# Kernel tuning notes

Hardware: AMD Instinct MI355X
Metric: run time of the kernel (lower is better)

## Reference

```python
import jax, jax.numpy as jnp
import numpy as np

H, I = 16, 64
SCALE = 1.0 / (I ** 0.5)

def _rel_shift(x):
    # x: (S, J, B, H) -> Transformer-XL relative shift trick
    S, J, B, Hh = x.shape
    pad = jnp.zeros((S, 1, B, Hh), dtype=x.dtype)
    y = jnp.concatenate([pad, x], axis=1)           # (S, J+1, B, H)
    y = y.reshape(J + 1, S, B, Hh)[1:]              # (J, S, B, H)
    return y.reshape(S, J, B, Hh)

def setup_inputs() -> dict:
    key = jax.random.key(0)
    ks = jax.random.split(key, 10)
    S, P, B, E = 1024, 1024, 4, 1024
    J = P + S
    # causal mask: query s may attend keys j <= P + s; True = blocked
    mask = (jnp.arange(J)[None, :] > (P + jnp.arange(S))[:, None])[..., None]  # (S,J,1) bool
    sc = E ** -0.5
    return {
        "inputMHA": jax.random.normal(ks[0], (S, B, E), jnp.float32),
        "posEmbeddings": jax.random.normal(ks[1], (J, E), jnp.float32),
        "memory": jax.random.normal(ks[2], (P, B, E), jnp.float32),
        "u": jax.random.normal(ks[3], (H, I), jnp.float32) * 0.02,
        "v": jax.random.normal(ks[4], (H, I), jnp.float32) * 0.02,
        "mask": mask,
        "W_kv": jax.random.normal(ks[5], (E, 2 * H * I), jnp.float32) * sc,
        "W_q": jax.random.normal(ks[6], (E, H * I), jnp.float32) * sc,
        "W_p": jax.random.normal(ks[7], (E, H * I), jnp.float32) * sc,
        "W_o": jax.random.normal(ks[8], (H * I, E), jnp.float32) * sc,
        "gamma": jnp.ones((E,), jnp.float32),
        "beta": jnp.zeros((E,), jnp.float32),
    }

def reference(inputMHA, posEmbeddings, memory, u, v, mask, W_kv, W_q, W_p, W_o, gamma, beta):
    S, B, E = inputMHA.shape
    P = memory.shape[0]
    J = P + S
    x = jnp.concatenate([memory, inputMHA], axis=0)          # (J,B,E)
    kv = x @ W_kv                                            # (J,B,2HI)
    keys, values = jnp.split(kv, 2, axis=-1)
    q = (inputMHA @ W_q).reshape(S, B, H, I)                 # (S,B,H,I)
    K = keys.reshape(J, B, H, I)
    content = jnp.einsum('sbhi,jbhi->sjbh', q + u, K)        # content score
    p = (posEmbeddings @ W_p).reshape(J, H, I)               # (J,H,I)
    pos = jnp.einsum('sbhi,jhi->sjbh', q + v, p)             # position score
    pos = _rel_shift(pos)
    attn = content + pos                                     # (S,J,B,H)
    attn = jnp.where(mask[..., None], -jnp.inf, attn)        # mask (S,J,1)->(S,J,1,1)
    attn = jax.nn.softmax(attn * jnp.asarray(SCALE, attn.dtype), axis=1)
    V = values.reshape(J, B, H, I)
    awv = jnp.einsum('sjbh,jbhi->sbhi', attn, V).reshape(S, B, H * I)
    out = inputMHA + awv @ W_o                               # residual (dropout = eval identity)
    mean = jnp.mean(out, axis=-1, keepdims=True)
    var = jnp.var(out, axis=-1, keepdims=True)
    return (out - mean) / jnp.sqrt(var + 1e-5) * gamma + beta
```

## Files before the change

### kernel.cpp

```cpp
#include <hip/hip_runtime.h>
#include <hip/hip_bf16.h>

#define S_ 1024
#define P_ 1024
#define B_ 4
#define E_ 1024
#define J_ 2048
#define H_ 16
#define I_ 64

typedef __bf16 bf16_t;
typedef __bf16 bf16x8 __attribute__((ext_vector_type(8)));
typedef __bf16 bf16x4 __attribute__((ext_vector_type(4)));
typedef unsigned short u16x8 __attribute__((ext_vector_type(8)));
typedef float f32x4 __attribute__((ext_vector_type(4)));

#define MFMA16(a, b, c) __builtin_amdgcn_mfma_f32_16x16x32_bf16(a, b, c, 0, 0, 0)

#define SWZ(r, c) (((r) << 6) + ((((((c) >> 3)) ^ ((r) & 7)) << 3)) + ((c) & 7))

__global__ __launch_bounds__(256) void cvt_all_kernel(const float* __restrict__ memory,
                                                      const float* __restrict__ input,
                                                      const float* __restrict__ posEmb,
                                                      bf16_t* __restrict__ Xbf,
                                                      bf16_t* __restrict__ Pemb) {
    int blk = blockIdx.x;
    const float* src;
    bf16_t* dst;
    if (blk < 4096) { src = memory; dst = Xbf; }
    else if (blk < 8192) { blk -= 4096; src = input; dst = Xbf + (size_t)P_ * B_ * E_; }
    else { blk -= 8192; src = posEmb; dst = Pemb; }
    int i = (blk * 256 + threadIdx.x) * 4;
    float4 v = *(const float4*)(src + i);
    bf16x4 o = {(bf16_t)v.x, (bf16_t)v.y, (bf16_t)v.z, (bf16_t)v.w};
    *(bf16x4*)(dst + i) = o;
}

__global__ void trans_all_kernel(const float* __restrict__ W_kv, bf16_t* __restrict__ Wkvt,
                                 const float* __restrict__ W_q, bf16_t* __restrict__ Wqt,
                                 const float* __restrict__ W_p, bf16_t* __restrict__ Wpt,
                                 const float* __restrict__ W_o, bf16_t* __restrict__ Wot) {
    __shared__ float tile[32][33];
    int z = blockIdx.z;
    const float* W = (z == 0) ? W_kv : (z == 1) ? W_q : (z == 2) ? W_p : W_o;
    bf16_t* Wt = (z == 0) ? Wkvt : (z == 1) ? Wqt : (z == 2) ? Wpt : Wot;
    int N = (z == 0) ? 2048 : 1024;
    if (blockIdx.x * 32 >= N) return;
    int n0 = blockIdx.x * 32, k0 = blockIdx.y * 32;
    int x = threadIdx.x, y = threadIdx.y;
    for (int i = 0; i < 32; i += 8)
        tile[y + i][x] = W[(size_t)(k0 + y + i) * N + n0 + x];
    __syncthreads();
    for (int i = 0; i < 32; i += 8)
        Wt[(size_t)(n0 + y + i) * 1024 + k0 + x] = (bf16_t)tile[x][y + i];
}

__device__ __forceinline__ void gemm_tile(
    const bf16_t* __restrict__ A, const bf16_t* __restrict__ Bt, int N,
    int m0, int n0, int epi,
    bf16_t* __restrict__ out0, bf16_t* __restrict__ out1,
    const float* __restrict__ add0, const float* __restrict__ add1,
    float* __restrict__ outf,
    bf16_t (*Al)[72], bf16_t (*Bl)[72]) {
    const int K = 1024;
    int tid = threadIdx.x;
    int wave = tid >> 6, lane = tid & 63, quad = lane >> 4, l16 = lane & 15;
    int wm = (wave & 1) * 64, wn = (wave >> 1) * 64;
    f32x4 zero = {0.f, 0.f, 0.f, 0.f};
    f32x4 acc[4][4];
    #pragma unroll
    for (int i = 0; i < 4; i++)
        #pragma unroll
        for (int j = 0; j < 4; j++) acc[i][j] = zero;

    for (int k0 = 0; k0 < K; k0 += 64) {
        __syncthreads();
        #pragma unroll
        for (int r = 0; r < 4; r++) {
            int idx = tid + 256 * r;
            int row = idx >> 3, seg = (idx & 7) * 8;
            *(uint4*)&Al[row][seg] = *(const uint4*)&A[(size_t)(m0 + row) * K + k0 + seg];
            *(uint4*)&Bl[row][seg] = *(const uint4*)&Bt[(size_t)(n0 + row) * K + k0 + seg];
        }
        __syncthreads();
        #pragma unroll
        for (int ks = 0; ks < 2; ks++) {
            bf16x8 af[4], bfr[4];
            #pragma unroll
            for (int i = 0; i < 4; i++)
                af[i] = *(const bf16x8*)&Al[wm + i * 16 + l16][ks * 32 + quad * 8];
            #pragma unroll
            for (int j = 0; j < 4; j++)
                bfr[j] = *(const bf16x8*)&Bl[wn + j * 16 + l16][ks * 32 + quad * 8];
            #pragma unroll
            for (int i = 0; i < 4; i++)
                #pragma unroll
                for (int j = 0; j < 4; j++) acc[i][j] = MFMA16(af[i], bfr[j], acc[i][j]);
        }
    }
    #pragma unroll
    for (int i = 0; i < 4; i++)
        #pragma unroll
        for (int j = 0; j < 4; j++)
            #pragma unroll
            for (int reg = 0; reg < 4; reg++) {
                int m = m0 + wm + i * 16 + quad * 4 + reg;
                int n = n0 + wn + j * 16 + l16;
                float v = acc[i][j][reg];
                if (epi == 0) {
                    out0[(size_t)m * N + n] = (bf16_t)v;
                } else if (epi == 1) {
                    out0[(size_t)m * N + n] = (bf16_t)(v + add0[n]);
                    out1[(size_t)m * N + n] = (bf16_t)(v + add1[n]);
                } else {
                    outf[(size_t)m * N + n] = v + add0[(size_t)m * N + n];
                }
            }
}

__global__ __launch_bounds__(256) void gemm3_kernel(
    const bf16_t* __restrict__ Xbf, const bf16_t* __restrict__ Wkvt, bf16_t* __restrict__ kvb,
    const bf16_t* __restrict__ Wqt, bf16_t* __restrict__ qub, bf16_t* __restrict__ qvb,
    const float* __restrict__ u, const float* __restrict__ v,
    const bf16_t* __restrict__ Pemb, const bf16_t* __restrict__ Wpt, bf16_t* __restrict__ pb) {
    __shared__ __attribute__((aligned(16))) bf16_t Al[128][72];
    __shared__ __attribute__((aligned(16))) bf16_t Bl[128][72];
    int id = blockIdx.x;
    if (id < 1024) {
        gemm_tile(Xbf, Wkvt, 2048, (id >> 4) * 128, (id & 15) * 128, 0,
                  kvb, nullptr, nullptr, nullptr, nullptr, Al, Bl);
    } else if (id < 1280) {
        int t = id - 1024;
        gemm_tile(Xbf + (size_t)P_ * B_ * E_, Wqt, 1024, (t >> 3) * 128, (t & 7) * 128, 1,
                  qub, qvb, u, v, nullptr, Al, Bl);
    } else {
        int t = id - 1280;
        gemm_tile(Pemb, Wpt, 1024, (t >> 3) * 128, (t & 7) * 128, 0,
                  pb, nullptr, nullptr, nullptr, nullptr, Al, Bl);
    }
}

__global__ __launch_bounds__(256) void gemmo_kernel(
    const bf16_t* __restrict__ awvb, const bf16_t* __restrict__ Wot,
    const float* __restrict__ inputMHA, float* __restrict__ opre) {
    __shared__ __attribute__((aligned(16))) bf16_t Al[128][72];
    __shared__ __attribute__((aligned(16))) bf16_t Bl[128][72];
    int id = blockIdx.x;
    gemm_tile(awvb, Wot, 1024, (id >> 3) * 128, (id & 7) * 128, 2,
              nullptr, nullptr, inputMHA, nullptr, opre, Al, Bl);
}

__global__ __launch_bounds__(256) void flash_kernel(
    const bf16_t* __restrict__ qu, const bf16_t* __restrict__ qv,
    const bf16_t* __restrict__ kv, const bf16_t* __restrict__ pm,
    float* __restrict__ Oacc, float* __restrict__ lacc) {
    __shared__ __attribute__((aligned(16))) bf16_t Klds[64 * 64];
    __shared__ __attribute__((aligned(16))) bf16_t Vt[64 * 64];
    __shared__ __attribute__((aligned(16))) bf16_t Plds[128 * 64];
    __shared__ __attribute__((aligned(16))) bf16_t Prob[4 * 16 * 64];

    int tid = threadIdx.x;
    int wave = tid >> 6, lane = tid & 63, quad = lane >> 4, l16 = lane & 15;

    int x = blockIdx.x;
    int s_blk, c;
    if (x < 24) { s_blk = x / 3; c = x - s_blk * 3; }
    else        { int y = x - 24; s_blk = 8 + (y >> 2); c = y & 3; }
    int nt = 17 + s_blk;
    int t0 = c * 8;
    int t1 = t0 + 8; if (t1 > nt) t1 = nt;

    int s0 = s_blk * 64;
    int bh = blockIdx.y;
    int b = bh >> 4, h = bh & 15;
    int srow0 = s0 + wave * 16;

    const bf16_t* qub = qu + ((size_t)(srow0 + l16) * B_ + b) * 1024 + h * 64 + quad * 8;
    const bf16_t* qvb = qv + ((size_t)(srow0 + l16) * B_ + b) * 1024 + h * 64 + quad * 8;
    bf16x8 aqu0 = *(const bf16x8*)(qub);
    bf16x8 aqu1 = *(const bf16x8*)(qub + 32);
    bf16x8 aqv0 = *(const bf16x8*)(qvb);
    bf16x8 aqv1 = *(const bf16x8*)(qvb + 32);

    f32x4 zero = {0.f, 0.f, 0.f, 0.f};
    f32x4 accO[4];
    #pragma unroll
    for (int ot = 0; ot < 4; ot++) accO[ot] = zero;
    float lrowp[4] = {0.f, 0.f, 0.f, 0.f};

    const int w0u = 960 - s0;
    const int woff = 48 - wave * 16;
    const float SCL = 0.125f * 1.44269504088896f;

    int jr = tid >> 3, seg8g = tid & 7;
    int jp = tid & 31, iseg = tid >> 5;
    uint* VtU = (uint*)&Vt[0];
    bf16_t* ProbW = Prob + (wave << 10);

    {
        int j0 = t0 * 64;
        const bf16_t* kp = kv + ((size_t)(j0 + jr) * B_ + b) * 2048 + h * 64 + seg8g * 8;
        uint4 ka = *(const uint4*)kp;
        uint4 kb = *(const uint4*)(kp + (size_t)32 * B_ * 2048);
        const bf16_t* vp = kv + ((size_t)(j0 + jp * 2) * B_ + b) * 2048 + 1024 + h * 64 + iseg * 8;
        u16x8 va = *(const u16x8*)vp;
        u16x8 vb = *(const u16x8*)(vp + (size_t)B_ * 2048);
        uint4 pd[4];
        #pragma unroll
        for (int r = 0; r < 4; r++) {
            int idx = tid + 256 * r;
            int pr = idx >> 3, pg = idx & 7;
            int lr = w0u + j0 + pr; if (lr > J_ - 1) lr = J_ - 1;
            pd[r] = *(const uint4*)(pm + (size_t)lr * 1024 + h * 64 + pg * 8);
        }
        *(uint4*)&Klds[SWZ(jr, seg8g * 8)] = ka;
        *(uint4*)&Klds[SWZ(jr + 32, seg8g * 8)] = kb;
        #pragma unroll
        for (int e = 0; e < 8; e++) {
            int row = iseg * 8 + e;
            VtU[(row << 5) + ((((jp >> 2) ^ (row & 7)) << 2)) + (jp & 3)] =
                (uint)va[e] | ((uint)vb[e] << 16);
        }
        #pragma unroll
        for (int r = 0; r < 4; r++) {
            int idx = tid + 256 * r;
            int pr = idx >> 3, pg = idx & 7;
            *(uint4*)&Plds[SWZ((w0u + j0 + pr) & 127, pg * 8)] = pd[r];
        }
    }
    __syncthreads();

    for (int it = t0; it < t1; it++) {
        int j0 = it * 64;
        bool pf = (it + 1 < t1);
        uint4 ka, kb, pd0, pd1;
        u16x8 va, vb;
        int pr0 = tid >> 3, pg0 = tid & 7;
        int pr1 = (tid + 256) >> 3, pg1 = tid & 7;
        if (pf) {
            int j1 = j0 + 64;
            const bf16_t* kp = kv + ((size_t)(j1 + jr) * B_ + b) * 2048 + h * 64 + seg8g * 8;
            ka = *(const uint4*)kp;
            kb = *(const uint4*)(kp + (size_t)32 * B_ * 2048);
            const bf16_t* vp = kv + ((size_t)(j1 + jp * 2) * B_ + b) * 2048 + 1024 + h * 64 + iseg * 8;
            va = *(const u16x8*)vp;
            vb = *(const u16x8*)(vp + (size_t)B_ * 2048);
            int lr0 = w0u + j0 + 128 + pr0; if (lr0 > J_ - 1) lr0 = J_ - 1;
            int lr1 = w0u + j0 + 128 + pr1; if (lr1 > J_ - 1) lr1 = J_ - 1;
            pd0 = *(const uint4*)(pm + (size_t)lr0 * 1024 + h * 64 + pg0 * 8);
            pd1 = *(const uint4*)(pm + (size_t)lr1 * 1024 + h * 64 + pg1 * 8);
        }

        f32x4 cs[4];
        #pragma unroll
        for (int t = 0; t < 4; t++) cs[t] = zero;
        #pragma unroll
        for (int ks = 0; ks < 2; ks++) {
            bf16x8 aq = ks ? aqu1 : aqu0;
            #pragma unroll
            for (int t = 0; t < 4; t++) {
                bf16x8 bk = *(const bf16x8*)&Klds[SWZ(t * 16 + l16, ks * 32 + quad * 8)];
                cs[t] = MFMA16(aq, bk, cs[t]);
            }
        }
        f32x4 ep[5];
        #pragma unroll
        for (int t = 0; t < 5; t++) ep[t] = zero;
        #pragma unroll
        for (int ks = 0; ks < 2; ks++) {
            bf16x8 aq = ks ? aqv1 : aqv0;
            #pragma unroll
            for (int t = 0; t < 5; t++) {
                int prow = (w0u + j0 + woff + t * 16 + l16) & 127;
                bf16x8 bp = *(const bf16x8*)&Plds[SWZ(prow, ks * 32 + quad * 8)];
                ep[t] = MFMA16(aq, bp, ep[t]);
            }
        }

        #pragma unroll
        for (int reg = 0; reg < 4; reg++) {
            int r = quad * 4 + reg;
            int s = srow0 + r;
            int idx = l16 + 15 - r;
            int srcl = quad * 16 + (idx & 15);
            float sh[5];
            #pragma unroll
            for (int t = 0; t < 5; t++) sh[t] = __shfl(ep[t][reg], srcl);
            float psum = 0.f;
            #pragma unroll
            for (int t = 0; t < 4; t++) {
                float pos = (idx < 16) ? sh[t] : sh[t + 1];
                float p = exp2f((cs[t][reg] + pos) * SCL);
                p = (j0 + t * 16 + l16 > P_ + s) ? 0.f : p;
                ProbW[SWZ(r, t * 16 + l16)] = (bf16_t)p;
                psum += p;
            }
            lrowp[reg] += psum;
        }

        #pragma unroll
        for (int ks = 0; ks < 2; ks++) {
            bf16x8 pa = *(const bf16x8*)&Prob[(wave << 10) + SWZ(l16, ks * 32 + quad * 8)];
            #pragma unroll
            for (int ot = 0; ot < 4; ot++) {
                bf16x8 bv = *(const bf16x8*)&Vt[SWZ(ot * 16 + l16, ks * 32 + quad * 8)];
                accO[ot] = MFMA16(pa, bv, accO[ot]);
            }
        }

        __syncthreads();
        if (pf) {
            *(uint4*)&Klds[SWZ(jr, seg8g * 8)] = ka;
            *(uint4*)&Klds[SWZ(jr + 32, seg8g * 8)] = kb;
            #pragma unroll
            for (int e2 = 0; e2 < 8; e2++) {
                int row = iseg * 8 + e2;
                VtU[(row << 5) + ((((jp >> 2) ^ (row & 7)) << 2)) + (jp & 3)] =
                    (uint)va[e2] | ((uint)vb[e2] << 16);
            }
            *(uint4*)&Plds[SWZ((w0u + j0 + pr0) & 127, pg0 * 8)] = pd0;
            *(uint4*)&Plds[SWZ((w0u + j0 + pr1) & 127, pg1 * 8)] = pd1;
        }
        __syncthreads();
    }

    #pragma unroll
    for (int reg = 0; reg < 4; reg++) {
        int r = quad * 4 + reg;
        int srow = srow0 + r;
        float l = lrowp[reg];
        #pragma unroll
        for (int d = 1; d < 16; d <<= 1) l += __shfl_xor(l, d);
        if (l16 == 0) atomicAdd(&lacc[((size_t)srow * B_ + b) * H_ + h], l);
        size_t rowoff = ((size_t)srow * B_ + b) * 1024 + h * 64;
        #pragma unroll
        for (int ot = 0; ot < 4; ot++)
            atomicAdd(&Oacc[rowoff + ot * 16 + l16], accO[ot][reg]);
    }
}

__global__ __launch_bounds__(256) void norm_kernel(const float* __restrict__ Oacc,
                                                   const float* __restrict__ lacc,
                                                   bf16_t* __restrict__ awv) {
    int i4 = (blockIdx.x * 256 + threadIdx.x) * 4;
    int row = i4 >> 6;
    float inv = 1.0f / lacc[row];
    float4 o = *(const float4*)(Oacc + i4);
    bf16x4 r = {(bf16_t)(o.x * inv), (bf16_t)(o.y * inv),
                (bf16_t)(o.z * inv), (bf16_t)(o.w * inv)};
    *(bf16x4*)(awv + i4) = r;
}

__global__ __launch_bounds__(256) void ln_kernel(const float* __restrict__ x,
                                                 const float* __restrict__ gamma,
                                                 const float* __restrict__ beta,
                                                 float* __restrict__ out) {
    int row = blockIdx.x, tid = threadIdx.x;
    int lane = tid & 63, wave = tid >> 6;
    float4 v = ((const float4*)(x + (size_t)row * 1024))[tid];
    float s = v.x + v.y + v.z + v.w;
    float ss = v.x * v.x + v.y * v.y + v.z * v.z + v.w * v.w;
    #pragma unroll
    for (int sh = 1; sh < 64; sh <<= 1) { s += __shfl_xor(s, sh); ss += __shfl_xor(ss, sh); }
    __shared__ float red[8];
    if (lane == 0) { red[wave] = s; red[4 + wave] = ss; }
    __syncthreads();
    s = red[0] + red[1] + red[2] + red[3];
    ss = red[4] + red[5] + red[6] + red[7];
    float mean = s * (1.f / 1024.f);
    float var = ss * (1.f / 1024.f) - mean * mean;
    float inv = rsqrtf(var + 1e-5f);
    float4 g = ((const float4*)gamma)[tid];
    float4 bt = ((const float4*)beta)[tid];
    float4 o;
    o.x = (v.x - mean) * inv * g.x + bt.x;
    o.y = (v.y - mean) * inv * g.y + bt.y;
    o.z = (v.z - mean) * inv * g.z + bt.z;
    o.w = (v.w - mean) * inv * g.w + bt.w;
    ((float4*)(out + (size_t)row * 1024))[tid] = o;
}

extern "C" void kernel_launch(void* const* d_in, const int* in_sizes, int n_in,
                              void* d_out, int out_size, void* d_ws, size_t ws_size,
                              hipStream_t stream) {
    const float* inputMHA = (const float*)d_in[0];
    const float* posEmb   = (const float*)d_in[1];
    const float* memory   = (const float*)d_in[2];
    const float* u        = (const float*)d_in[3];
    const float* v        = (const float*)d_in[4];
    const float* W_kv     = (const float*)d_in[6];
    const float* W_q      = (const float*)d_in[7];
    const float* W_p      = (const float*)d_in[8];
    const float* W_o      = (const float*)d_in[9];
    const float* gamma    = (const float*)d_in[10];
    const float* beta     = (const float*)d_in[11];
    float* out = (float*)d_out;

    char* ws = (char*)d_ws;
    size_t off = 0;
    auto alloc = [&](size_t bytes) -> void* {
        void* p = ws + off;
        off += (bytes + 255) & ~(size_t)255;
        return p;
    };
    bf16_t* Xbf  = (bf16_t*)alloc((size_t)J_ * B_ * E_ * 2);
    bf16_t* Wkvt = (bf16_t*)alloc((size_t)2048 * 1024 * 2);
    bf16_t* Wqt  = (bf16_t*)alloc((size_t)1024 * 1024 * 2);
    bf16_t* Wpt  = (bf16_t*)alloc((size_t)1024 * 1024 * 2);
    bf16_t* Wot  = (bf16_t*)alloc((size_t)1024 * 1024 * 2);
    bf16_t* Pemb = (bf16_t*)alloc((size_t)2048 * 1024 * 2);
    bf16_t* kvb  = (bf16_t*)alloc((size_t)8192 * 2048 * 2);
    bf16_t* qub  = (bf16_t*)alloc((size_t)4096 * 1024 * 2);
    bf16_t* qvb  = (bf16_t*)alloc((size_t)4096 * 1024 * 2);
    bf16_t* pb   = (bf16_t*)alloc((size_t)2048 * 1024 * 2);
    bf16_t* awvb = (bf16_t*)alloc((size_t)4096 * 1024 * 2);
    float*  opre = (float*)alloc((size_t)4096 * 1024 * 4);
    float*  Oacc = (float*)alloc((size_t)4096 * 1024 * 4);
    float*  lacc = (float*)alloc((size_t)S_ * B_ * H_ * 4);

    hipMemsetAsync(Oacc, 0, (size_t)4096 * 1024 * 4, stream);
    hipMemsetAsync(lacc, 0, (size_t)S_ * B_ * H_ * 4, stream);

    cvt_all_kernel<<<10240, 256, 0, stream>>>(memory, inputMHA, posEmb, Xbf, Pemb);
    trans_all_kernel<<<dim3(64, 32, 4), dim3(32, 8), 0, stream>>>(
        W_kv, Wkvt, W_q, Wqt, W_p, Wpt, W_o, Wot);

    gemm3_kernel<<<1408, 256, 0, stream>>>(Xbf, Wkvt, kvb, Wqt, qub, qvb, u, v, Pemb, Wpt, pb);

    flash_kernel<<<dim3(56, B_ * H_), 256, 0, stream>>>(qub, qvb, kvb, pb, Oacc, lacc);
    norm_kernel<<<4096, 256, 0, stream>>>(Oacc, lacc, awvb);

    gemmo_kernel<<<256, 256, 0, stream>>>(awvb, Wot, inputMHA, opre);
    ln_kernel<<<S_ * B_, 256, 0, stream>>>(opre, gamma, beta, out);
}
```

Baseline: 444.5 us.

## Precompute relative-shifted position scores in a separate kernel before flash attention

Adds a pos_kernel that computes the (q+v)·p position scores for all query/key tiles and writes them, already relative-shifted and laid out per lane, into a large bf16 workspace buffer. A new flash_pos_kernel then reads these scores instead of recomputing the five position MFMAs and lane shuffles per tile inside the attention loop. Both kernels also raise wave priority around the MFMA sections. The trade is a round trip of roughly half a gigabyte of extra global memory traffic in exchange for less compute and shuffle work in the flash loop. It falls back to half-batch launches or the old kernel depending on workspace size.

After: 521.3 us. 1.17x slower.

```diff
diff --git a/kernel.cpp b/kernel.cpp
--- a/kernel.cpp
+++ b/kernel.cpp
@@ -150,7 +150,215 @@
               nullptr, nullptr, inputMHA, nullptr, opre, Al, Bl);
 }
 
-__global__ __launch_bounds__(256) void flash_kernel(
+__global__ __launch_bounds__(256) void pos_kernel(
+    const bf16_t* __restrict__ qv, const bf16_t* __restrict__ pb,
+    bf16_t* __restrict__ pos, int boff) {
+    int tid = threadIdx.x;
+    int wave = tid >> 6, lane = tid & 63, quad = lane >> 4, l16 = lane & 15;
+    int s_blk = blockIdx.x;
+    int bh = blockIdx.y;
+    int b = boff + (bh >> 4), h = bh & 15;
+    int srow0 = s_blk * 64 + wave * 16;
+
+    const bf16_t* qp = qv + ((size_t)(srow0 + l16) * B_ + b) * 1024 + h * 64 + quad * 8;
+    bf16x8 a0 = *(const bf16x8*)qp;
+    bf16x8 a1 = *(const bf16x8*)(qp + 32);
+
+    int st = s_blk * 4 + wave;
+    int jthi = (17 + s_blk) * 4;
+    size_t base = ((size_t)bh << 21) + ((size_t)st << 15);
+    int jtb[4];
+    int lowoff[4];
+    #pragma unroll
+    for (int reg = 0; reg < 4; reg++) {
+        int s = srow0 + quad * 4 + reg;
+        int base_r = l16 + s - 1023;
+        jtb[reg] = base_r >> 4;
+        int jlow = base_r & 15;
+        lowoff[reg] = (quad * 16 + jlow) * 4 + reg;
+    }
+    const bf16_t* pbh = pb + h * 64;
+
+    for (int kt = 0; kt < 32; kt++) {
+        int k0 = kt * 64;
+        f32x4 cs[4];
+        #pragma unroll
+        for (int t = 0; t < 4; t++) {
+            const bf16_t* pp = pbh + (size_t)(k0 + t * 16 + l16) * 1024 + quad * 8;
+            bf16x8 b0 = *(const bf16x8*)pp;
+            bf16x8 b1 = *(const bf16x8*)(pp + 32);
+            f32x4 z = {0.f, 0.f, 0.f, 0.f};
+            cs[t] = MFMA16(a1, b1, MFMA16(a0, b0, z));
+        }
+        #pragma unroll
+        for (int t = 0; t < 4; t++)
+            #pragma unroll
+            for (int reg = 0; reg < 4; reg++) {
+                int jt = jtb[reg] + kt * 4 + t;
+                if (jt >= 0 && jt < jthi)
+                    pos[base + ((size_t)jt << 8) + lowoff[reg]] = (bf16_t)cs[t][reg];
+            }
+    }
+}
+
+__global__ __launch_bounds__(256) void flash_pos_kernel(
+    const bf16_t* __restrict__ qu,
+    const bf16_t* __restrict__ kv, const bf16_t* __restrict__ pos,
+    float* __restrict__ Oacc, float* __restrict__ lacc, int boff) {
+    __shared__ __attribute__((aligned(16))) bf16_t Klds[64 * 64];
+    __shared__ __attribute__((aligned(16))) bf16_t Vt[64 * 64];
+    __shared__ __attribute__((aligned(16))) bf16_t Prob[4 * 16 * 64];
+
+    int tid = threadIdx.x;
+    int wave = tid >> 6, lane = tid & 63, quad = lane >> 4, l16 = lane & 15;
+
+    int x = blockIdx.x;
+    int s_blk, c;
+    if (x < 24) { s_blk = x / 3; c = x - s_blk * 3; }
+    else        { int y = x - 24; s_blk = 8 + (y >> 2); c = y & 3; }
+    int nt = 17 + s_blk;
+    int t0 = c * 8;
+    int t1 = t0 + 8; if (t1 > nt) t1 = nt;
+
+    int s0 = s_blk * 64;
+    int bh = blockIdx.y;
+    int b = boff + (bh >> 4), h = bh & 15;
+    int srow0 = s0 + wave * 16;
+
+    const bf16_t* qub = qu + ((size_t)(srow0 + l16) * B_ + b) * 1024 + h * 64 + quad * 8;
+    bf16x8 aqu0 = *(const bf16x8*)(qub);
+    bf16x8 aqu1 = *(const bf16x8*)(qub + 32);
+
+    const bf16_t* posb = pos + ((size_t)bh << 21) + ((size_t)(s_blk * 4 + wave) << 15) + lane * 4;
+
+    f32x4 zero = {0.f, 0.f, 0.f, 0.f};
+    f32x4 accO[4];
+    #pragma unroll
+    for (int ot = 0; ot < 4; ot++) accO[ot] = zero;
+    float lrowp[4] = {0.f, 0.f, 0.f, 0.f};
+
+    const float SCL = 0.125f * 1.44269504088896f;
+
+    int jr = tid >> 3, seg8g = tid & 7;
+    int jp = tid & 31, iseg = tid >> 5;
+    uint* VtU = (uint*)&Vt[0];
+    bf16_t* ProbW = Prob + (wave << 10);
+
+    bf16x4 pq[4], pqn[4];
+    {
+        int j0 = t0 * 64;
+        const bf16_t* kp = kv + ((size_t)(j0 + jr) * B_ + b) * 2048 + h * 64 + seg8g * 8;
+        uint4 ka = *(const uint4*)kp;
+        uint4 kb = *(const uint4*)(kp + (size_t)32 * B_ * 2048);
+        const bf16_t* vp = kv + ((size_t)(j0 + jp * 2) * B_ + b) * 2048 + 1024 + h * 64 + iseg * 8;
+        u16x8 va = *(const u16x8*)vp;
+        u16x8 vb = *(const u16x8*)(vp + (size_t)B_ * 2048);
+        #pragma unroll
+        for (int t = 0; t < 4; t++)
+            pq[t] = *(const bf16x4*)(posb + ((size_t)(t0 * 4 + t) << 8));
+        *(uint4*)&Klds[SWZ(jr, seg8g * 8)] = ka;
+        *(uint4*)&Klds[SWZ(jr + 32, seg8g * 8)] = kb;
+        #pragma unroll
+        for (int e = 0; e < 8; e++) {
+            int row = iseg * 8 + e;
+            VtU[(row << 5) + ((((jp >> 2) ^ (row & 7)) << 2)) + (jp & 3)] =
+                (uint)va[e] | ((uint)vb[e] << 16);
+        }
+    }
+    __syncthreads();
+
+    for (int it = t0; it < t1; it++) {
+        int j0 = it * 64;
+        bool pf = (it + 1 < t1);
+        uint4 ka, kb;
+        u16x8 va, vb;
+        if (pf) {
+            int j1 = j0 + 64;
+            const bf16_t* kp = kv + ((size_t)(j1 + jr) * B_ + b) * 2048 + h * 64 + seg8g * 8;
+            ka = *(const uint4*)kp;
+            kb = *(const uint4*)(kp + (size_t)32 * B_ * 2048);
+            const bf16_t* vp = kv + ((size_t)(j1 + jp * 2) * B_ + b) * 2048 + 1024 + h * 64 + iseg * 8;
+            va = *(const u16x8*)vp;
+            vb = *(const u16x8*)(vp + (size_t)B_ * 2048);
+            #pragma unroll
+            for (int t = 0; t < 4; t++)
+                pqn[t] = *(const bf16x4*)(posb + ((size_t)((it + 1) * 4 + t) << 8));
+        }
+
+        f32x4 cs[4];
+        #pragma unroll
+        for (int t = 0; t < 4; t++) cs[t] = zero;
+        __builtin_amdgcn_s_setprio(1);
+        #pragma unroll
+        for (int ks = 0; ks < 2; ks++) {
+            bf16x8 aq = ks ? aqu1 : aqu0;
+            #pragma unroll
+            for (int t = 0; t < 4; t++) {
+                bf16x8 bk = *(const bf16x8*)&Klds[SWZ(t * 16 + l16, ks * 32 + quad * 8)];
+                cs[t] = MFMA16(aq, bk, cs[t]);
+            }
+        }
+        __builtin_amdgcn_s_setprio(0);
+
+        #pragma unroll
+        for (int reg = 0; reg < 4; reg++) {
+            int r = quad * 4 + reg;
+            int s = srow0 + r;
+            float psum = 0.f;
+            #pragma unroll
+            for (int t = 0; t < 4; t++) {
+                float p = exp2f((cs[t][reg] + (float)pq[t][reg]) * SCL);
+                p = (j0 + t * 16 + l16 > P_ + s) ? 0.f : p;
+                ProbW[SWZ(r, t * 16 + l16)] = (bf16_t)p;
+                psum += p;
+            }
+            lrowp[reg] += psum;
+        }
+
+        __builtin_amdgcn_s_setprio(1);
+        #pragma unroll
+        for (int ks = 0; ks < 2; ks++) {
+            bf16x8 pa = *(const bf16x8*)&Prob[(wave << 10) + SWZ(l16, ks * 32 + quad * 8)];
+            #pragma unroll
+            for (int ot = 0; ot < 4; ot++) {
+                bf16x8 bv = *(const bf16x8*)&Vt[SWZ(ot * 16 + l16, ks * 32 + quad * 8)];
+                accO[ot] = MFMA16(pa, bv, accO[ot]);
+            }
+        }
+        __builtin_amdgcn_s_setprio(0);
+
+        __syncthreads();
+        if (pf) {
+            *(uint4*)&Klds[SWZ(jr, seg8g * 8)] = ka;
+            *(uint4*)&Klds[SWZ(jr + 32, seg8g * 8)] = kb;
+            #pragma unroll
+            for (int e2 = 0; e2 < 8; e2++) {
+                int row = iseg * 8 + e2;
+                VtU[(row << 5) + ((((jp >> 2) ^ (row & 7)) << 2)) + (jp & 3)] =
+                    (uint)va[e2] | ((uint)vb[e2] << 16);
+            }
+            #pragma unroll
+            for (int t = 0; t < 4; t++) pq[t] = pqn[t];
+        }
+        __syncthreads();
+    }
+
+    #pragma unroll
+    for (int reg = 0; reg < 4; reg++) {
+        int r = quad * 4 + reg;
+        int srow = srow0 + r;
+        float l = lrowp[reg];
+        #pragma unroll
+        for (int d = 1; d < 16; d <<= 1) l += __shfl_xor(l, d);
+        if (l16 == 0) atomicAdd(&lacc[((size_t)srow * B_ + b) * H_ + h], l);
+        size_t rowoff = ((size_t)srow * B_ + b) * 1024 + h * 64;
+        #pragma unroll
+        for (int ot = 0; ot < 4; ot++)
+            atomicAdd(&Oacc[rowoff + ot * 16 + l16], accO[ot][reg]);
+    }
+}
+
+__global__ __launch_bounds__(256) void flash_old_kernel(
     const bf16_t* __restrict__ qu, const bf16_t* __restrict__ qv,
     const bf16_t* __restrict__ kv, const bf16_t* __restrict__ pm,
     float* __restrict__ Oacc, float* __restrict__ lacc) {
@@ -254,6 +462,7 @@
         f32x4 cs[4];
         #pragma unroll
         for (int t = 0; t < 4; t++) cs[t] = zero;
+        __builtin_amdgcn_s_setprio(1);
         #pragma unroll
         for (int ks = 0; ks < 2; ks++) {
             bf16x8 aq = ks ? aqu1 : aqu0;
@@ -276,6 +485,7 @@
                 ep[t] = MFMA16(aq, bp, ep[t]);
             }
         }
+        __builtin_amdgcn_s_setprio(0);
 
         #pragma unroll
         for (int reg = 0; reg < 4; reg++) {
@@ -298,6 +508,7 @@
             lrowp[reg] += psum;
         }
 
+        __builtin_amdgcn_s_setprio(1);
         #pragma unroll
         for (int ks = 0; ks < 2; ks++) {
             bf16x8 pa = *(const bf16x8*)&Prob[(wave << 10) + SWZ(l16, ks * 32 + quad * 8)];
@@ -307,6 +518,7 @@
                 accO[ot] = MFMA16(pa, bv, accO[ot]);
             }
         }
+        __builtin_amdgcn_s_setprio(0);
 
         __syncthreads();
         if (pf) {
@@ -417,6 +629,10 @@
     float*  opre = (float*)alloc((size_t)4096 * 1024 * 4);
     float*  Oacc = (float*)alloc((size_t)4096 * 1024 * 4);
     float*  lacc = (float*)alloc((size_t)S_ * B_ * H_ * 4);
+    size_t base_end = off;
+
+    const size_t POS_FULL = (size_t)64 * 64 * 128 * 256 * 2;
+    const size_t POS_HALF = POS_FULL / 2;
 
     hipMemsetAsync(Oacc, 0, (size_t)4096 * 1024 * 4, stream);
     hipMemsetAsync(lacc, 0, (size_t)S_ * B_ * H_ * 4, stream);
@@ -427,7 +643,20 @@
 
     gemm3_kernel<<<1408, 256, 0, stream>>>(Xbf, Wkvt, kvb, Wqt, qub, qvb, u, v, Pemb, Wpt, pb);
 
-    flash_kernel<<<dim3(56, B_ * H_), 256, 0, stream>>>(qub, qvb, kvb, pb, Oacc, lacc);
+    if (ws_size >= base_end + POS_FULL + 256) {
+        bf16_t* posS = (bf16_t*)alloc(POS_FULL);
+        pos_kernel<<<dim3(16, 64), 256, 0, stream>>>(qvb, pb, posS, 0);
+        flash_pos_kernel<<<dim3(56, 64), 256, 0, stream>>>(qub, kvb, posS, Oacc, lacc, 0);
+    } else if (ws_size >= base_end + POS_HALF + 256) {
+        bf16_t* posS = (bf16_t*)alloc(POS_HALF);
+        for (int boff = 0; boff < 4; boff += 2) {
+            pos_kernel<<<dim3(16, 32), 256, 0, stream>>>(qvb, pb, posS, boff);
+            flash_pos_kernel<<<dim3(56, 32), 256, 0, stream>>>(qub, kvb, posS, Oacc, lacc, boff);
+        }
+    } else {
+        flash_old_kernel<<<dim3(56, B_ * H_), 256, 0, stream>>>(qub, qvb, kvb, pb, Oacc, lacc);
+    }
+
     norm_kernel<<<4096, 256, 0, stream>>>(Oacc, lacc, awvb);
 
     gemmo_kernel<<<256, 256, 0, stream>>>(awvb, Wot, inputMHA, opre);
```

## Load positional-embedding tiles directly into registers and add MFMA wave priority

Applied to the files above, without the earlier changes.

The flash kernel no longer stages the projected position embeddings through a 128-row shared-memory ring. Each wave now loads its own 80-row window of pb straight from global memory into registers, one load per tile iteration, and feeds those registers to the position-score MFMAs. This frees 16KB of LDS and drops the LDS writes and swizzled reads for P. The cost is that loads are no longer shared across the four waves (more global/L2 traffic) and the load latency is exposed, because these loads are issued in the same iteration they are consumed. s_setprio is also raised around the MFMA blocks to favour matrix issue.

After: 503.3 us. +13.2%, slower.

```diff
diff --git a/kernel.cpp b/kernel.cpp
--- a/kernel.cpp
+++ b/kernel.cpp
@@ -150,13 +150,12 @@
               nullptr, nullptr, inputMHA, nullptr, opre, Al, Bl);
 }
 
-__global__ __launch_bounds__(256) void flash_kernel(
+__global__ __launch_bounds__(256) void flash_fused_kernel(
     const bf16_t* __restrict__ qu, const bf16_t* __restrict__ qv,
-    const bf16_t* __restrict__ kv, const bf16_t* __restrict__ pm,
+    const bf16_t* __restrict__ kv, const bf16_t* __restrict__ pb,
     float* __restrict__ Oacc, float* __restrict__ lacc) {
     __shared__ __attribute__((aligned(16))) bf16_t Klds[64 * 64];
     __shared__ __attribute__((aligned(16))) bf16_t Vt[64 * 64];
-    __shared__ __attribute__((aligned(16))) bf16_t Plds[128 * 64];
     __shared__ __attribute__((aligned(16))) bf16_t Prob[4 * 16 * 64];
 
     int tid = threadIdx.x;
@@ -188,14 +187,14 @@
     for (int ot = 0; ot < 4; ot++) accO[ot] = zero;
     float lrowp[4] = {0.f, 0.f, 0.f, 0.f};
 
-    const int w0u = 960 - s0;
-    const int woff = 48 - wave * 16;
+    const int dbase = 1008 - srow0;
     const float SCL = 0.125f * 1.44269504088896f;
 
     int jr = tid >> 3, seg8g = tid & 7;
     int jp = tid & 31, iseg = tid >> 5;
     uint* VtU = (uint*)&Vt[0];
     bf16_t* ProbW = Prob + (wave << 10);
+    const bf16_t* pbh = pb + h * 64 + quad * 8;
 
     {
         int j0 = t0 * 64;
@@ -205,14 +204,6 @@
         const bf16_t* vp = kv + ((size_t)(j0 + jp * 2) * B_ + b) * 2048 + 1024 + h * 64 + iseg * 8;
         u16x8 va = *(const u16x8*)vp;
         u16x8 vb = *(const u16x8*)(vp + (size_t)B_ * 2048);
-        uint4 pd[4];
-        #pragma unroll
-        for (int r = 0; r < 4; r++) {
-            int idx = tid + 256 * r;
-            int pr = idx >> 3, pg = idx & 7;
-            int lr = w0u + j0 + pr; if (lr > J_ - 1) lr = J_ - 1;
-            pd[r] = *(const uint4*)(pm + (size_t)lr * 1024 + h * 64 + pg * 8);
-        }
         *(uint4*)&Klds[SWZ(jr, seg8g * 8)] = ka;
         *(uint4*)&Klds[SWZ(jr + 32, seg8g * 8)] = kb;
         #pragma unroll
@@ -221,22 +212,25 @@
             VtU[(row << 5) + ((((jp >> 2) ^ (row & 7)) << 2)) + (jp & 3)] =
                 (uint)va[e] | ((uint)vb[e] << 16);
         }
-        #pragma unroll
-        for (int r = 0; r < 4; r++) {
-            int idx = tid + 256 * r;
-            int pr = idx >> 3, pg = idx & 7;
-            *(uint4*)&Plds[SWZ((w0u + j0 + pr) & 127, pg * 8)] = pd[r];
-        }
     }
     __syncthreads();
 
     for (int it = t0; it < t1; it++) {
         int j0 = it * 64;
         bool pf = (it + 1 < t1);
-        uint4 ka, kb, pd0, pd1;
+
+        bf16x8 bp0[5], bp1[5];
+        #pragma unroll
+        for (int t = 0; t < 5; t++) {
+            int d = j0 + dbase + t * 16 + l16;
+            if (d > J_ - 1) d = J_ - 1;
+            const bf16_t* pp = pbh + (size_t)d * 1024;
+            bp0[t] = *(const bf16x8*)pp;
+            bp1[t] = *(const bf16x8*)(pp + 32);
+        }
+
+        uint4 ka, kb;
         u16x8 va, vb;
-        int pr0 = tid >> 3, pg0 = tid & 7;
-        int pr1 = (tid + 256) >> 3, pg1 = tid & 7;
         if (pf) {
             int j1 = j0 + 64;
             const bf16_t* kp = kv + ((size_t)(j1 + jr) * B_ + b) * 2048 + h * 64 + seg8g * 8;
@@ -245,15 +239,12 @@
             const bf16_t* vp = kv + ((size_t)(j1 + jp * 2) * B_ + b) * 2048 + 1024 + h * 64 + iseg * 8;
             va = *(const u16x8*)vp;
             vb = *(const u16x8*)(vp + (size_t)B_ * 2048);
-            int lr0 = w0u + j0 + 128 + pr0; if (lr0 > J_ - 1) lr0 = J_ - 1;
-            int lr1 = w0u + j0 + 128 + pr1; if (lr1 > J_ - 1) lr1 = J_ - 1;
-            pd0 = *(const uint4*)(pm + (size_t)lr0 * 1024 + h * 64 + pg0 * 8);
-            pd1 = *(const uint4*)(pm + (size_t)lr1 * 1024 + h * 64 + pg1 * 8);
         }
 
         f32x4 cs[4];
         #pragma unroll
         for (int t = 0; t < 4; t++) cs[t] = zero;
+        __builtin_amdgcn_s_setprio(1);
         #pragma unroll
         for (int ks = 0; ks < 2; ks++) {
             bf16x8 aq = ks ? aqu1 : aqu0;
@@ -265,17 +256,9 @@
         }
         f32x4 ep[5];
         #pragma unroll
-        for (int t = 0; t < 5; t++) ep[t] = zero;
-        #pragma unroll
-        for (int ks = 0; ks < 2; ks++) {
-            bf16x8 aq = ks ? aqv1 : aqv0;
-            #pragma unroll
-            for (int t = 0; t < 5; t++) {
-                int prow = (w0u + j0 + woff + t * 16 + l16) & 127;
-                bf16x8 bp = *(const bf16x8*)&Plds[SWZ(prow, ks * 32 + quad * 8)];
-                ep[t] = MFMA16(aq, bp, ep[t]);
-            }
-        }
+        for (int t = 0; t < 5; t++)
+            ep[t] = MFMA16(aqv1, bp1[t], MFMA16(aqv0, bp0[t], zero));
+        __builtin_amdgcn_s_setprio(0);
 
         #pragma unroll
         for (int reg = 0; reg < 4; reg++) {
@@ -298,6 +281,7 @@
             lrowp[reg] += psum;
         }
 
+        __builtin_amdgcn_s_setprio(1);
         #pragma unroll
         for (int ks = 0; ks < 2; ks++) {
             bf16x8 pa = *(const bf16x8*)&Prob[(wave << 10) + SWZ(l16, ks * 32 + quad * 8)];
@@ -307,6 +291,7 @@
                 accO[ot] = MFMA16(pa, bv, accO[ot]);
             }
         }
+        __builtin_amdgcn_s_setprio(0);
 
         __syncthreads();
         if (pf) {
@@ -318,8 +303,6 @@
                 VtU[(row << 5) + ((((jp >> 2) ^ (row & 7)) << 2)) + (jp & 3)] =
                     (uint)va[e2] | ((uint)vb[e2] << 16);
             }
-            *(uint4*)&Plds[SWZ((w0u + j0 + pr0) & 127, pg0 * 8)] = pd0;
-            *(uint4*)&Plds[SWZ((w0u + j0 + pr1) & 127, pg1 * 8)] = pd1;
         }
         __syncthreads();
     }
@@ -427,7 +410,7 @@
 
     gemm3_kernel<<<1408, 256, 0, stream>>>(Xbf, Wkvt, kvb, Wqt, qub, qvb, u, v, Pemb, Wpt, pb);
 
-    flash_kernel<<<dim3(56, B_ * H_), 256, 0, stream>>>(qub, qvb, kvb, pb, Oacc, lacc);
+    flash_fused_kernel<<<dim3(56, B_ * H_), 256, 0, stream>>>(qub, qvb, kvb, pb, Oacc, lacc);
     norm_kernel<<<4096, 256, 0, stream>>>(Oacc, lacc, awvb);
 
     gemmo_kernel<<<256, 256, 0, stream>>>(awvb, Wot, inputMHA, opre);
```
